# Performance work log

Hardware: AMD Instinct MI355X
Metric: run time of the kernel (lower is better)

The kernel has to match this reference:

```python
import jax, jax.numpy as jnp
import numpy as np

D = 32          # latent_dimension
N = 100000      # num nodes
E = 3200000     # num edges (avg degree 32)
K = 4           # message-passing steps
GAMMA = 0.9
ALPHA = 0.5


def _lin(key, out_f, in_f):
    s = 1.0 / np.sqrt(in_f)
    kw, kb = jax.random.split(key)
    W = jax.random.uniform(kw, (out_f, in_f), minval=-s, maxval=s, dtype=jnp.float32)
    b = jax.random.uniform(kb, (out_f,), minval=-s, maxval=s, dtype=jnp.float32)
    return W, b


def setup_inputs() -> dict:
    key = jax.random.key(0)
    k = iter(jax.random.split(key, 32))
    inp = {}
    inp['x'] = jax.random.normal(next(k), (N, 3), dtype=jnp.float32)
    inp['y'] = jax.random.normal(next(k), (N, 2), dtype=jnp.float32)
    inp['edge_index'] = jax.random.randint(next(k), (2, E), 0, N)
    inp['edge_attr'] = jax.random.uniform(next(k), (E, 2), dtype=jnp.float32)
    inp['to_W1'], inp['to_b1'] = _lin(next(k), D, 2 * D + 2)
    inp['to_W2'], inp['to_b2'] = _lin(next(k), D, D)
    inp['fr_W1'], inp['fr_b1'] = _lin(next(k), D, 2 * D + 2)
    inp['fr_W2'], inp['fr_b2'] = _lin(next(k), D, D)
    inp['lp_W1'], inp['lp_b1'] = _lin(next(k), D, 2 * D + 1)
    inp['lp_W2'], inp['lp_b2'] = _lin(next(k), D, D)
    inp['gru_Wih'], inp['gru_bih'] = _lin(next(k), 3 * D, 4 * D + 3)
    inp['gru_Whh'], inp['gru_bhh'] = _lin(next(k), 3 * D, D)
    inp['dec_W1'], inp['dec_b1'] = _lin(next(k), D, D)
    inp['dec_W2'], inp['dec_b2'] = _lin(next(k), 2, D)
    return inp


def _mlp2(h, W1, b1, W2, b2):
    return jax.nn.relu(h @ W1.T + b1) @ W2.T + b2


def reference(x, y, edge_index, edge_attr,
              to_W1, to_b1, to_W2, to_b2,
              fr_W1, fr_b1, fr_W2, fr_b2,
              lp_W1, lp_b1, lp_W2, lp_b2,
              gru_Wih, gru_bih, gru_Whh, gru_bhh,
              dec_W1, dec_b1, dec_W2, dec_b2):
    n = x.shape[0]
    d = gru_Whh.shape[1]
    src, dst = edge_index[0], edge_index[1]
    nonself = src != dst                     # remove_self_loops in Phi modules
    emask = nonself.astype(x.dtype)          # [E]

    # Loop module: add_self_loops(weight=1), adjacency diagonal = 1 + sum of
    # original self-loop weights (edge_attr[:,0]); loop_col = 1 - diag.
    diag = jnp.ones((n,), x.dtype).at[src].add(
        jnp.where(nonself, jnp.zeros_like(edge_attr[:, 0]), edge_attr[:, 0]))
    loop_col = (1.0 - diag)[:, None]         # [N,1]

    def agg_mean(msg, idx):
        # masked scatter-mean over edges -> nodes; nodes w/o messages get 0
        s = jax.ops.segment_sum(msg * emask[:, None], idx, num_segments=n)
        c = jax.ops.segment_sum(emask, idx, num_segments=n)
        return s / jnp.maximum(c, 1.0)[:, None]

    def gru_step(xin):  # single-step GRU, h0 = 0 (W_hh @ h vanishes)
        g = xin @ gru_Wih.T + gru_bih
        r_x, z_x, n_x = jnp.split(g, 3, axis=-1)
        b_hr, b_hz, b_hn = jnp.split(gru_bhh, 3)
        r = jax.nn.sigmoid(r_x + b_hr)
        z = jax.nn.sigmoid(z_x + b_hz)
        nn_ = jnp.tanh(n_x + r * b_hn)
        return (1.0 - z) * nn_

    def decode(H):
        return _mlp2(H, dec_W1, dec_b1, dec_W2, dec_b2)

    H = jnp.zeros((n, d), x.dtype)
    losses = []
    F = decode(H)
    for _ in range(K):
        h_dst, h_src = H[dst], H[src]
        # Phi_to: flow source_to_target -> x_i = x[dst], x_j = x[src], agg @ dst
        m_to = agg_mean(_mlp2(jnp.concatenate([h_dst, h_src, edge_attr], 1),
                              to_W1, to_b1, to_W2, to_b2), dst)
        # Phi_from: flow target_to_source -> x_i = x[src], x_j = x[dst], agg @ src
        m_fr = agg_mean(_mlp2(jnp.concatenate([h_src, h_dst, edge_attr], 1),
                              fr_W1, fr_b1, fr_W2, fr_b2), src)
        lp = _mlp2(jnp.concatenate([H, H, loop_col], 1), lp_W1, lp_b1, lp_W2, lp_b2)
        concat = jnp.concatenate([H, m_to, m_fr, lp, x], 1)   # [N, 4D+3]
        H = gru_step(concat) * ALPHA + H
        F = decode(H)
        losses.append(jnp.mean((F - y) ** 2))
    losses = jnp.stack(losses)                                # [K]
    weights = GAMMA ** jnp.arange(K - 1, -1, -1, dtype=x.dtype)
    total_loss = jnp.sum(losses * weights)
    return F, total_loss, losses
```

## Files before the change

kernel.cpp:

```cpp
#include <hip/hip_runtime.h>
#include <math.h>


#define BSHIFT 9
#define BIN_W 512
#define CAP 17408
#define EPB 8192

__device__ __forceinline__ unsigned int pack_bf(float x) {
  unsigned int u = __float_as_uint(x);
  u += 0x7fffu + ((u >> 16) & 1u);
  return u >> 16;
}

__global__ void combine_kernel(const float* __restrict__ Wih, const float* __restrict__ bih,
    const float* __restrict__ toW2, const float* __restrict__ tob2,
    const float* __restrict__ frW2, const float* __restrict__ frb2,
    const float* __restrict__ lpW2, const float* __restrict__ lpb2,
    const float* __restrict__ lpW1,
    float* __restrict__ Wg, float* __restrict__ Wlp1c) {
  int tid = blockIdx.x * blockDim.x + threadIdx.x;
  if (tid < 9216) {
    int seg = tid / 3072, r2 = tid % 3072, g = r2 >> 5, j = r2 & 31;
    const float* W2 = seg == 0 ? toW2 : (seg == 1 ? frW2 : lpW2);
    const float* wrow = Wih + g*131 + 32 + seg*32;
    float s = 0.f;
    #pragma unroll
    for (int k = 0; k < 32; k++) s += wrow[k] * W2[k*32 + j];
    int nr = (g & 31)*3 + (g >> 5);
    Wg[nr*136 + 32 + seg*32 + j] = s;
  } else if (tid < 12288) {
    int r2 = tid - 9216, g = r2 >> 5, k = r2 & 31;
    int nr = (g & 31)*3 + (g >> 5);
    Wg[nr*136 + k] = Wih[g*131 + k];
  } else if (tid < 12576) {
    int r2 = tid - 12288; int g = r2 / 3, c = r2 % 3;
    int nr = (g & 31)*3 + (g >> 5);
    Wg[nr*136 + 128 + c] = Wih[g*131 + 128 + c];
  } else if (tid < 12672) {
    int g = tid - 12576;
    float vt = 0.f, vf = 0.f, bl = 0.f;
    #pragma unroll
    for (int k = 0; k < 32; k++) {
      vt += Wih[g*131 + 32 + k] * tob2[k];
      vf += Wih[g*131 + 64 + k] * frb2[k];
      bl += Wih[g*131 + 96 + k] * lpb2[k];
    }
    int nr = (g & 31)*3 + (g >> 5);
    Wg[nr*136 + 131] = bih[g] + bl;
    Wg[nr*136 + 132] = vt;
    Wg[nr*136 + 133] = vf;
  } else if (tid < 13696) {
    int r2 = tid - 12672; int i = r2 >> 5, k = r2 & 31;
    Wlp1c[i*32 + k] = lpW1[i*65 + k] + lpW1[i*65 + 32 + k];
  }
}

__global__ __launch_bounds__(256) void transpose_kernel(
    const float* __restrict__ Wg, const float* __restrict__ toW1,
    const float* __restrict__ frW1, const float* __restrict__ Wlp1c,
    const float* __restrict__ lpW1, const float* __restrict__ lpb1,
    float* __restrict__ Wgt, float* __restrict__ Wc, float* __restrict__ Wtail) {
  int tid = blockIdx.x*256 + threadIdx.x;
  if (tid < 12864) {
    int og = tid / 1608, r = tid % 1608, k = r / 12, jj = r % 12;
    Wgt[(og*134 + k)*16 + jj] = Wg[(og*12 + jj)*136 + k];
  } else if (tid < 12864 + 5120) {
    int r = tid - 12864;
    int og = r / 640, r2 = r % 640, k = r2 / 20, j = r2 % 20;
    int f = og*4 + (j & 3);
    int cls = j >> 2;
    float v;
    if      (cls == 0) v = toW1[f*66 + k];
    else if (cls == 1) v = toW1[f*66 + 32 + k];
    else if (cls == 2) v = frW1[f*66 + k];
    else if (cls == 3) v = frW1[f*66 + 32 + k];
    else               v = Wlp1c[f*32 + k];
    Wc[(og*32 + k)*24 + j] = v;
  } else if (tid < 12864 + 5120 + 64) {
    int f = tid - 12864 - 5120;
    Wtail[f] = (f < 32) ? lpW1[f*65 + 64] : lpb1[f - 32];
  }
}

__global__ __launch_bounds__(1024) void scatter_bin_kernel(
    const int* __restrict__ ei, const float* __restrict__ ea,
    int* __restrict__ cursor_to, int* __restrict__ cursor_fr,
    uint2* __restrict__ binned_to, uint2* __restrict__ binned_fr,
    float* __restrict__ loop_col, int E) {
  __shared__ int lh_to[256], lh_fr[256];
  __shared__ int gb_to[256], gb_fr[256];
  int t = threadIdx.x;
  if (t < 256) { lh_to[t] = 0; lh_fr[t] = 0; }
  __syncthreads();
  int base_e = blockIdx.x * EPB;
  #pragma unroll
  for (int j = 0; j < EPB/1024; j++) {
    int e = base_e + j*1024 + t;
    if (e < E) {
      int ss = ei[e], dd = ei[E + e];
      if (ss != dd) {
        atomicAdd(&lh_to[dd >> BSHIFT], 1);
        atomicAdd(&lh_fr[ss >> BSHIFT], 1);
      } else {
        atomicAdd(&loop_col[ss], -ea[2*e]);
      }
    }
  }
  __syncthreads();
  if (t < 256) {
    int c = lh_to[t]; gb_to[t] = c ? atomicAdd(&cursor_to[t], c) : 0; lh_to[t] = 0;
    c = lh_fr[t];     gb_fr[t] = c ? atomicAdd(&cursor_fr[t], c) : 0; lh_fr[t] = 0;
  }
  __syncthreads();
  #pragma unroll
  for (int j = 0; j < EPB/1024; j++) {
    int e = base_e + j*1024 + t;
    if (e < E) {
      int ss = ei[e], dd = ei[E + e];
      if (ss != dd) {
        float2 a = ((const float2*)ea)[e];
        unsigned int ep = pack_bf(a.x) | (pack_bf(a.y) << 16);
        int bt = dd >> BSHIFT, bf = ss >> BSHIFT;
        int st = gb_to[bt] + atomicAdd(&lh_to[bt], 1);
        int sf = gb_fr[bf] + atomicAdd(&lh_fr[bf], 1);
        if (st < CAP) binned_to[(size_t)bt*CAP + st] =
            make_uint2((unsigned int)ss | ((unsigned int)(dd & 511) << 17), ep);
        if (sf < CAP) binned_fr[(size_t)bf*CAP + sf] =
            make_uint2((unsigned int)dd | ((unsigned int)(ss & 511) << 17), ep);
      }
    }
  }
}

__global__ __launch_bounds__(256) void bin_count_kernel(
    const uint2* __restrict__ binned_to, const int* __restrict__ cursor_to,
    const uint2* __restrict__ binned_fr, const int* __restrict__ cursor_fr,
    int* __restrict__ cnt_dst, int* __restrict__ cnt_src, int NB, int N) {
  __shared__ int c[BIN_W];
  int b = blockIdx.x;
  bool second = b >= NB;
  if (second) b -= NB;
  const uint2* binned = second ? binned_fr : binned_to;
  const int* cursor   = second ? cursor_fr : cursor_to;
  int* cnt            = second ? cnt_src   : cnt_dst;
  for (int i = threadIdx.x; i < BIN_W; i += 256) c[i] = 0;
  __syncthreads();
  int m = cursor[b]; if (m > CAP) m = CAP;
  const uint2* seg = binned + (size_t)b*CAP;
  for (int i = threadIdx.x; i < m; i += 256)
    atomicAdd(&c[seg[i].x >> 17], 1);
  __syncthreads();
  for (int i = threadIdx.x; i < BIN_W; i += 256) {
    int n = (b << BSHIFT) + i;
    if (n < N) cnt[n] = c[i];
  }
}

__global__ __launch_bounds__(256) void scan_part_kernel(
    const int* __restrict__ cnt_a, const int* __restrict__ cnt_b,
    int* __restrict__ part, int n, int G) {
  __shared__ int ws[4];
  int b = blockIdx.x, t = threadIdx.x, lane = t & 63, w = t >> 6;
  int base = b*1024 + t*4;
  for (int which = 0; which < 2; which++) {
    const int* cnt = which ? cnt_b : cnt_a;
    int sum = 0;
    #pragma unroll
    for (int j = 0; j < 4; j++) if (base + j < n) sum += cnt[base + j];
    #pragma unroll
    for (int off = 32; off; off >>= 1) sum += __shfl_down(sum, off, 64);
    if (lane == 0) ws[w] = sum;
    __syncthreads();
    if (t == 0) part[which*G + b] = ws[0] + ws[1] + ws[2] + ws[3];
    __syncthreads();
  }
}

__global__ __launch_bounds__(256) void scan_mid_kernel(
    int* __restrict__ part, int* __restrict__ row_a, int* __restrict__ row_b,
    int n, int G) {
  __shared__ int ws[2][4];
  int t = threadIdx.x, lane = t & 63, w = t >> 6;
  for (int which = 0; which < 2; which++) {
    int v = (t < G) ? part[which*G + t] : 0;
    int orig = v;
    #pragma unroll
    for (int off = 1; off < 64; off <<= 1) {
      int u = __shfl_up(v, off, 64);
      if (lane >= off) v += u;
    }
    if (lane == 63) ws[which][w] = v;
    __syncthreads();
    int wadd = 0;
    for (int i = 0; i < w; i++) wadd += ws[which][i];
    int incl = v + wadd;
    if (t < G) part[which*G + t] = incl - orig;
    if (t == G - 1) { int* row = which ? row_b : row_a; row[n] = incl; }
    __syncthreads();
  }
}

__global__ __launch_bounds__(256) void scan_apply_kernel(
    const int* __restrict__ cnt_a, const int* __restrict__ cnt_b,
    const int* __restrict__ part, int* __restrict__ row_a, int* __restrict__ row_b,
    int n, int G) {
  __shared__ int ws[4];
  int b = blockIdx.x, t = threadIdx.x, lane = t & 63, w = t >> 6;
  int base = b*1024 + t*4;
  for (int which = 0; which < 2; which++) {
    const int* cnt = which ? cnt_b : cnt_a;
    int* row = which ? row_b : row_a;
    int v0 = (base   < n) ? cnt[base]   : 0;
    int v1 = (base+1 < n) ? cnt[base+1] : 0;
    int v2 = (base+2 < n) ? cnt[base+2] : 0;
    int v3 = (base+3 < n) ? cnt[base+3] : 0;
    int tsum = v0 + v1 + v2 + v3;
    int v = tsum;
    #pragma unroll
    for (int off = 1; off < 64; off <<= 1) {
      int u = __shfl_up(v, off, 64);
      if (lane >= off) v += u;
    }
    if (lane == 63) ws[w] = v;
    __syncthreads();
    int wadd = 0;
    for (int i = 0; i < w; i++) wadd += ws[i];
    int excl = v - tsum + wadd + part[which*G + b];
    if (base   < n) row[base]   = excl;
    if (base+1 < n) row[base+1] = excl + v0;
    if (base+2 < n) row[base+2] = excl + v0 + v1;
    if (base+3 < n) row[base+3] = excl + v0 + v1 + v2;
    __syncthreads();
  }
}

__global__ __launch_bounds__(256) void place_kernel(
    const uint2* __restrict__ binned_to, const int* __restrict__ cursor_to,
    const uint2* __restrict__ binned_fr, const int* __restrict__ cursor_fr,
    const int* __restrict__ row_to, const int* __restrict__ row_fr,
    uint2* __restrict__ rec_to, uint2* __restrict__ rec_fr, int NB, int N) {
  __shared__ int cur[BIN_W];
  int b = blockIdx.x;
  bool second = b >= NB;
  if (second) b -= NB;
  const uint2* binned = second ? binned_fr : binned_to;
  const int* cursor   = second ? cursor_fr : cursor_to;
  const int* row      = second ? row_fr    : row_to;
  uint2* rec          = second ? rec_fr    : rec_to;
  int n0 = b << BSHIFT;
  for (int i = threadIdx.x; i < BIN_W; i += 256) {
    int n = n0 + i;
    cur[i] = (n < N) ? row[n] : 0;
  }
  __syncthreads();
  int m = cursor[b]; if (m > CAP) m = CAP;
  const uint2* seg = binned + (size_t)b*CAP;
  for (int i = threadIdx.x; i < m; i += 256) {
    uint2 r = seg[i];
    int pos = atomicAdd(&cur[r.x >> 17], 1);
    rec[pos] = make_uint2((r.x & 0x1ffffu) << 6, r.y);
  }
}

__global__ __launch_bounds__(256) void hlp0_kernel(
    const float* __restrict__ lpW1, const float* __restrict__ lpb1,
    const float* __restrict__ loop_col, float* __restrict__ inX, int N) {
  int tid = blockIdx.x*256 + threadIdx.x;
  int n = tid >> 5, f = tid & 31;
  if (n < N)
    inX[(size_t)n*128 + 96 + f] = fmaxf(lpW1[f*65 + 64]*loop_col[n] + lpb1[f], 0.f);
}

__global__ __launch_bounds__(256) void agg_dual_kernel(
    const float* __restrict__ Pti, const unsigned short* __restrict__ Ptj,
    const int* __restrict__ row_to, const uint2* __restrict__ rec_to,
    const float* __restrict__ toW1, const float* __restrict__ tob1,
    const float* __restrict__ Pfi, const unsigned short* __restrict__ Pfj,
    const int* __restrict__ row_fr, const uint2* __restrict__ rec_fr,
    const float* __restrict__ frW1, const float* __restrict__ frb1,
    float* __restrict__ inX, int skipP, int N) {
  int b = blockIdx.x;
  int low = b & 7;
  bool second = low >= 4;
  int inner = (b >> 3)*4 + (low & 3);
  const float* Pi            = second ? Pfi   : Pti;
  const unsigned short* Pj   = second ? Pfj   : Ptj;
  const int* row             = second ? row_fr: row_to;
  const uint2* rec           = second ? rec_fr: rec_to;
  const float* W1            = second ? frW1  : toW1;
  const float* b1            = second ? frb1  : tob1;
  int slot                   = second ? 64    : 32;
  int t = inner*256 + threadIdx.x;
  int n = t >> 5;
  if (n >= N) return;
  int f = t & 31;
  int start = row[n], end = row[n+1];
  float we0 = W1[f*66 + 64], we1 = W1[f*66 + 65];
  float s = 0.f;
  const char* Pjb = (const char*)Pj;
  unsigned f2 = (unsigned)(f << 1);
  if (skipP) {
    float base = b1[f];
    int i = start;
    if ((i & 1) && i < end) {
      unsigned ep = rec[i].y;
      float e0 = __uint_as_float(ep << 16);
      float e1 = __uint_as_float(ep & 0xffff0000u);
      s += fmaxf(base + we0*e0 + we1*e1, 0.f);
      i++;
    }
    int npair = (end - i) >> 1;
    const uint4* rp4 = (const uint4*)(rec + i);
    #pragma unroll 4
    for (int p = 0; p < npair; p++) {
      uint4 rr = *rp4++;
      float e0a = __uint_as_float(rr.y << 16);
      float e1a = __uint_as_float(rr.y & 0xffff0000u);
      s += fmaxf(base + we0*e0a + we1*e1a, 0.f);
      float e0b = __uint_as_float(rr.w << 16);
      float e1b = __uint_as_float(rr.w & 0xffff0000u);
      s += fmaxf(base + we0*e0b + we1*e1b, 0.f);
    }
    i += npair << 1;
    if (i < end) {
      unsigned ep = rec[i].y;
      float e0 = __uint_as_float(ep << 16);
      float e1 = __uint_as_float(ep & 0xffff0000u);
      s += fmaxf(base + we0*e0 + we1*e1, 0.f);
    }
  } else {
    float base = Pi[n*32 + f] + b1[f];
    int i = start;
    if ((i & 1) && i < end) {
      uint2 r = rec[i];
      float e0 = __uint_as_float(r.y << 16);
      float e1 = __uint_as_float(r.y & 0xffff0000u);
      unsigned pv = *(const unsigned short*)(Pjb + (r.x + f2));
      float pj = __uint_as_float(pv << 16);
      s += fmaxf(base + pj + we0*e0 + we1*e1, 0.f);
      i++;
    }
    int npair = (end - i) >> 1;
    const uint4* rp4 = (const uint4*)(rec + i);
    #pragma unroll 4
    for (int p = 0; p < npair; p++) {
      uint4 rr = *rp4++;
      unsigned pva = *(const unsigned short*)(Pjb + (rr.x + f2));
      unsigned pvb = *(const unsigned short*)(Pjb + (rr.z + f2));
      float e0a = __uint_as_float(rr.y << 16);
      float e1a = __uint_as_float(rr.y & 0xffff0000u);
      float pja = __uint_as_float(pva << 16);
      s += fmaxf(base + pja + we0*e0a + we1*e1a, 0.f);
      float e0b = __uint_as_float(rr.w << 16);
      float e1b = __uint_as_float(rr.w & 0xffff0000u);
      float pjb_ = __uint_as_float(pvb << 16);
      s += fmaxf(base + pjb_ + we0*e0b + we1*e1b, 0.f);
    }
    i += npair << 1;
    if (i < end) {
      uint2 r = rec[i];
      float e0 = __uint_as_float(r.y << 16);
      float e1 = __uint_as_float(r.y & 0xffff0000u);
      unsigned pv = *(const unsigned short*)(Pjb + (r.x + f2));
      float pj = __uint_as_float(pv << 16);
      s += fmaxf(base + pj + we0*e0 + we1*e1, 0.f);
    }
  }
  int c = end - start;
  inX[(size_t)n*128 + slot + f] = s / (float)(c > 0 ? c : 1);
}

__global__ __launch_bounds__(512, 8) void node_update_kernel(
    float* __restrict__ inX, const float* __restrict__ Wgt,
    const float* __restrict__ x, const float* __restrict__ y,
    const int* __restrict__ cnt_dst, const int* __restrict__ cnt_src,
    const float* __restrict__ bhh,
    const float* __restrict__ dW1, const float* __restrict__ db1,
    const float* __restrict__ dW2, const float* __restrict__ db2,
    const float* __restrict__ loop_col,
    const float* __restrict__ Wc, const float* __restrict__ Wtail,
    float* __restrict__ Pti, unsigned short* __restrict__ Ptj,
    float* __restrict__ Pfi, unsigned short* __restrict__ Pfj,
    float* __restrict__ Fout, float* __restrict__ loss_acc, int k_iter, int N) {
  __shared__ float sbuf[64*137];
  __shared__ float sF[1024];
  int t = threadIdx.x;
  int node0 = blockIdx.x * 64;
  {
    const float4* src = (const float4*)(inX + (size_t)node0*128);
    int nvalid = N - node0; if (nvalid > 64) nvalid = 64;
    int nfl4 = nvalid * 32;
    for (int i = t; i < 64*32; i += 512) {
      float4 v = (i < nfl4) ? src[i] : make_float4(0.f, 0.f, 0.f, 0.f);
      int node = i >> 5, k = (i & 31) * 4;
      float* dp = &sbuf[node*137 + k];
      dp[0] = v.x; dp[1] = v.y; dp[2] = v.z; dp[3] = v.w;
    }
    if (t < 64) {
      int n = node0 + t;
      float x0=0.f, x1=0.f, x2=0.f, gt=0.f, gf=0.f;
      if (n < N) {
        x0 = x[n*3]; x1 = x[n*3+1]; x2 = x[n*3+2];
        gt = cnt_dst[n] > 0 ? 1.f : 0.f;
        gf = cnt_src[n] > 0 ? 1.f : 0.f;
      }
      float* dp = &sbuf[t*137 + 128];
      dp[0]=x0; dp[1]=x1; dp[2]=x2; dp[3]=1.f; dp[4]=gt; dp[5]=gf;
    }
  }
  __syncthreads();
  int lane_node = t & 63;
  int og = __builtin_amdgcn_readfirstlane(t >> 6);
  const float* inrow = &sbuf[lane_node*137];
  float acc[12];
  #pragma unroll
  for (int jj = 0; jj < 12; jj++) acc[jj] = 0.f;
  const float* wt = Wgt + og*134*16;
  #pragma unroll 4
  for (int k = 0; k < 134; k++) {
    float iv = inrow[k];
    const float* wk = wt + k*16;
    #pragma unroll
    for (int jj = 0; jj < 12; jj++) acc[jj] += wk[jj] * iv;
  }
  float hnew[4];
  {
    int n = node0 + lane_node;
    #pragma unroll
    for (int q = 0; q < 4; q++) {
      int f = og*4 + q;
      float r = 1.f/(1.f + __expf(-(acc[q*3]   + bhh[f])));
      float z = 1.f/(1.f + __expf(-(acc[q*3+1] + bhh[32+f])));
      float nn = tanhf(acc[q*3+2] + r*bhh[64+f]);
      hnew[q] = (1.f - z)*nn*0.5f + inrow[f];
      if (n < N) inX[(size_t)n*128 + f] = hnew[q];
    }
  }
  __syncthreads();
  #pragma unroll
  for (int q = 0; q < 4; q++) sbuf[lane_node*137 + og*4 + q] = hnew[q];
  __syncthreads();
  float F0p = 0.f, F1p = 0.f;
  #pragma unroll
  for (int q = 0; q < 4; q++) {
    int jd = og*4 + q;
    float a = db1[jd];
    const float* wd = dW1 + jd*32;
    #pragma unroll
    for (int k = 0; k < 32; k++) a += wd[k]*inrow[k];
    a = fmaxf(a, 0.f);
    F0p += dW2[jd]*a;
    F1p += dW2[32+jd]*a;
  }
  sF[t*2] = F0p; sF[t*2+1] = F1p;
  __syncthreads();
  if (k_iter < 3) {
    int n = node0 + lane_node;
    bool valid = n < N;
    float lc = valid ? loop_col[n] : 0.f;
    int fb = og*4;
    float a[20];
    #pragma unroll
    for (int j = 0; j < 20; j++) a[j] = 0.f;
    const float* wc = Wc + og*32*24;
    #pragma unroll 2
    for (int k = 0; k < 32; k++) {
      float hk = inrow[k];
      const float* wck = wc + k*24;
      #pragma unroll
      for (int j = 0; j < 20; j++) a[j] += wck[j] * hk;
    }
    if (valid) {
      *(float4*)&Pti[(size_t)n*32 + fb] = make_float4(a[0],a[1],a[2],a[3]);
      uint2 u;
      u.x = pack_bf(a[4]) | (pack_bf(a[5]) << 16);
      u.y = pack_bf(a[6]) | (pack_bf(a[7]) << 16);
      *(uint2*)&Ptj[(size_t)n*32 + fb] = u;
      *(float4*)&Pfi[(size_t)n*32 + fb] = make_float4(a[8],a[9],a[10],a[11]);
      u.x = pack_bf(a[12]) | (pack_bf(a[13]) << 16);
      u.y = pack_bf(a[14]) | (pack_bf(a[15]) << 16);
      *(uint2*)&Pfj[(size_t)n*32 + fb] = u;
      float hl[4];
      #pragma unroll
      for (int q = 0; q < 4; q++)
        hl[q] = fmaxf(a[16+q] + Wtail[fb+q]*lc + Wtail[32+fb+q], 0.f);
      *(float4*)&inX[(size_t)n*128 + 96 + fb] = make_float4(hl[0],hl[1],hl[2],hl[3]);
    }
  }
  float my_loss = 0.f;
  if (og == 0) {
    int n = node0 + lane_node;
    float F0 = db2[0], F1 = db2[1];
    #pragma unroll
    for (int w = 0; w < 8; w++) {
      F0 += sF[(t + 64*w)*2];
      F1 += sF[(t + 64*w)*2 + 1];
    }
    if (n < N) {
      ((float2*)Fout)[n] = make_float2(F0, F1);
      float e0 = F0 - y[n*2], e1 = F1 - y[n*2+1];
      my_loss = e0*e0 + e1*e1;
    }
  }
  #pragma unroll
  for (int off = 32; off > 0; off >>= 1) my_loss += __shfl_down(my_loss, off, 64);
  if (t == 0) atomicAdd(&loss_acc[k_iter], my_loss);
}

__global__ void finalize_kernel(const float* __restrict__ loss_acc, float* __restrict__ out, int N) {
  if (threadIdx.x == 0 && blockIdx.x == 0) {
    float inv = 1.f/(2.f*(float)N);
    float l0 = loss_acc[0]*inv, l1 = loss_acc[1]*inv, l2 = loss_acc[2]*inv, l3 = loss_acc[3]*inv;
    out[0] = l0*0.729f + l1*0.81f + l2*0.9f + l3;
    out[1] = l0; out[2] = l1; out[3] = l2; out[4] = l3;
  }
}

extern "C" void kernel_launch(void* const* d_in, const int* in_sizes, int n_in,
                              void* d_out, int out_size, void* d_ws, size_t ws_size,
                              hipStream_t stream) {
  const float* x    = (const float*)d_in[0];
  const float* y    = (const float*)d_in[1];
  const int*   ei   = (const int*)  d_in[2];
  const float* ea   = (const float*)d_in[3];
  const float* toW1 = (const float*)d_in[4];  const float* tob1 = (const float*)d_in[5];
  const float* toW2 = (const float*)d_in[6];  const float* tob2 = (const float*)d_in[7];
  const float* frW1 = (const float*)d_in[8];  const float* frb1 = (const float*)d_in[9];
  const float* frW2 = (const float*)d_in[10]; const float* frb2 = (const float*)d_in[11];
  const float* lpW1 = (const float*)d_in[12]; const float* lpb1 = (const float*)d_in[13];
  const float* lpW2 = (const float*)d_in[14]; const float* lpb2 = (const float*)d_in[15];
  const float* gWih = (const float*)d_in[16]; const float* gbih = (const float*)d_in[17];
  const float* gbhh = (const float*)d_in[19];
  const float* dW1  = (const float*)d_in[20]; const float* db1  = (const float*)d_in[21];
  const float* dW2  = (const float*)d_in[22]; const float* db2  = (const float*)d_in[23];
  const int N = in_sizes[0] / 3;
  const int E = in_sizes[3] / 2;
  const int NB = (N + BIN_W - 1) >> BSHIFT;
  const int G  = (N + 1023) >> 10;

  char* p = (char*)d_ws;
  auto carve = [&](size_t bytes) -> void* {
    void* r = (void*)p;
    p += (bytes + 255) & ~(size_t)255;
    return r;
  };
  float* inX       = (float*)carve((size_t)N*128*4);
  float* loop_col  = (float*)carve((size_t)N*4);
  int*   cursor_to = (int*)  carve((size_t)NB*4);
  int*   cursor_fr = (int*)  carve((size_t)NB*4);
  float* loss_acc  = (float*)carve(64);
  size_t zero_bytes = (size_t)(p - (char*)d_ws);
  int*    row_to   = (int*)  carve((size_t)(N+1)*4);
  int*    row_fr   = (int*)  carve((size_t)(N+1)*4);
  int*    cnt_dst  = (int*)  carve((size_t)N*4);
  int*    cnt_src  = (int*)  carve((size_t)N*4);
  int*    part     = (int*)  carve((size_t)2*G*4);
  uint2*  binned_to= (uint2*)carve((size_t)NB*CAP*8);
  uint2*  binned_fr= (uint2*)carve((size_t)NB*CAP*8);
  uint2*  rec_to   = (uint2*)carve((size_t)E*8);
  uint2*  rec_fr   = (uint2*)carve((size_t)E*8);
  float*  Pti      = (float*)carve((size_t)N*32*4);
  float*  Pfi      = (float*)carve((size_t)N*32*4);
  unsigned short* Ptj = (unsigned short*)carve((size_t)N*32*2);
  unsigned short* Pfj = (unsigned short*)carve((size_t)N*32*2);
  float*  Wg       = (float*)carve((size_t)96*136*4);
  float*  Wlp1c    = (float*)carve(32*32*4);
  float*  Wgt      = (float*)carve((size_t)8*134*16*4);
  float*  Wc       = (float*)carve((size_t)8*32*24*4);
  float*  Wtail    = (float*)carve(64*4);

  hipMemsetAsync(d_ws, 0, zero_bytes, stream);
  combine_kernel<<<54, 256, 0, stream>>>(gWih, gbih, toW2, tob2, frW2, frb2, lpW2, lpb2,
                                         lpW1, Wg, Wlp1c);
  transpose_kernel<<<71, 256, 0, stream>>>(Wg, toW1, frW1, Wlp1c, lpW1, lpb1,
                                           Wgt, Wc, Wtail);
  scatter_bin_kernel<<<(E+EPB-1)/EPB, 1024, 0, stream>>>(ei, ea, cursor_to, cursor_fr,
                                                         binned_to, binned_fr, loop_col, E);
  bin_count_kernel<<<2*NB, 256, 0, stream>>>(binned_to, cursor_to, binned_fr, cursor_fr,
                                             cnt_dst, cnt_src, NB, N);
  scan_part_kernel<<<G, 256, 0, stream>>>(cnt_dst, cnt_src, part, N, G);
  scan_mid_kernel<<<1, 256, 0, stream>>>(part, row_to, row_fr, N, G);
  scan_apply_kernel<<<G, 256, 0, stream>>>(cnt_dst, cnt_src, part, row_to, row_fr, N, G);
  place_kernel<<<2*NB, 256, 0, stream>>>(binned_to, cursor_to, binned_fr, cursor_fr,
                                         row_to, row_fr, rec_to, rec_fr, NB, N);
  hlp0_kernel<<<(N*32 + 255)/256, 256, 0, stream>>>(lpW1, lpb1, loop_col, inX, N);

  float* Fout     = (float*)d_out;
  float* loss_out = (float*)d_out + (size_t)N*2;

  int aggHalf = (N*32 + 255)/256;
  int aggHalf4 = (aggHalf + 3) & ~3;
  for (int k = 0; k < 4; k++) {
    agg_dual_kernel<<<2*aggHalf4, 256, 0, stream>>>(Pti, Ptj, row_to, rec_to, toW1, tob1,
                                                    Pfi, Pfj, row_fr, rec_fr, frW1, frb1,
                                                    inX, (k == 0) ? 1 : 0, N);
    node_update_kernel<<<(N+63)/64, 512, 0, stream>>>(inX, Wgt, x, y,
        cnt_dst, cnt_src, gbhh, dW1, db1, dW2, db2,
        loop_col, Wc, Wtail,
        Pti, Ptj, Pfi, Pfj, Fout, loss_acc, k, N);
  }
  finalize_kernel<<<1, 64, 0, stream>>>(loss_acc, loss_out, N);
}
```

Baseline: 1.021 ms.

## Fuse edge aggregation into node update kernel with double-buffered projections

Merges the separate per-iteration aggregation kernel into the node update kernel, so each block gathers messages for its 64 nodes directly into shared memory instead of writing them to inX and reading them back. Because blocks now read neighbour projections while other blocks write new ones, the projection buffers are double-buffered, with the second set carved out of the no-longer-needed binning scratch space. This removes a launch and the inX round trip per iteration. The cost is less parallelism for the gather: 16 warps per block walk 4 nodes each serially, and register or occupancy pressure in one large kernel may rise.

Measured after the change: 1.069 ms. +4.8%, slower.

```diff
diff --git a/kernel.cpp b/kernel.cpp
--- a/kernel.cpp
+++ b/kernel.cpp
@@ -272,106 +272,7 @@
     inX[(size_t)n*128 + 96 + f] = fmaxf(lpW1[f*65 + 64]*loop_col[n] + lpb1[f], 0.f);
 }
 
-__global__ __launch_bounds__(256) void agg_dual_kernel(
-    const float* __restrict__ Pti, const unsigned short* __restrict__ Ptj,
-    const int* __restrict__ row_to, const uint2* __restrict__ rec_to,
-    const float* __restrict__ toW1, const float* __restrict__ tob1,
-    const float* __restrict__ Pfi, const unsigned short* __restrict__ Pfj,
-    const int* __restrict__ row_fr, const uint2* __restrict__ rec_fr,
-    const float* __restrict__ frW1, const float* __restrict__ frb1,
-    float* __restrict__ inX, int skipP, int N) {
-  int b = blockIdx.x;
-  int low = b & 7;
-  bool second = low >= 4;
-  int inner = (b >> 3)*4 + (low & 3);
-  const float* Pi            = second ? Pfi   : Pti;
-  const unsigned short* Pj   = second ? Pfj   : Ptj;
-  const int* row             = second ? row_fr: row_to;
-  const uint2* rec           = second ? rec_fr: rec_to;
-  const float* W1            = second ? frW1  : toW1;
-  const float* b1            = second ? frb1  : tob1;
-  int slot                   = second ? 64    : 32;
-  int t = inner*256 + threadIdx.x;
-  int n = t >> 5;
-  if (n >= N) return;
-  int f = t & 31;
-  int start = row[n], end = row[n+1];
-  float we0 = W1[f*66 + 64], we1 = W1[f*66 + 65];
-  float s = 0.f;
-  const char* Pjb = (const char*)Pj;
-  unsigned f2 = (unsigned)(f << 1);
-  if (skipP) {
-    float base = b1[f];
-    int i = start;
-    if ((i & 1) && i < end) {
-      unsigned ep = rec[i].y;
-      float e0 = __uint_as_float(ep << 16);
-      float e1 = __uint_as_float(ep & 0xffff0000u);
-      s += fmaxf(base + we0*e0 + we1*e1, 0.f);
-      i++;
-    }
-    int npair = (end - i) >> 1;
-    const uint4* rp4 = (const uint4*)(rec + i);
-    #pragma unroll 4
-    for (int p = 0; p < npair; p++) {
-      uint4 rr = *rp4++;
-      float e0a = __uint_as_float(rr.y << 16);
-      float e1a = __uint_as_float(rr.y & 0xffff0000u);
-      s += fmaxf(base + we0*e0a + we1*e1a, 0.f);
-      float e0b = __uint_as_float(rr.w << 16);
-      float e1b = __uint_as_float(rr.w & 0xffff0000u);
-      s += fmaxf(base + we0*e0b + we1*e1b, 0.f);
-    }
-    i += npair << 1;
-    if (i < end) {
-      unsigned ep = rec[i].y;
-      float e0 = __uint_as_float(ep << 16);
-      float e1 = __uint_as_float(ep & 0xffff0000u);
-      s += fmaxf(base + we0*e0 + we1*e1, 0.f);
-    }
-  } else {
-    float base = Pi[n*32 + f] + b1[f];
-    int i = start;
-    if ((i & 1) && i < end) {
-      uint2 r = rec[i];
-      float e0 = __uint_as_float(r.y << 16);
-      float e1 = __uint_as_float(r.y & 0xffff0000u);
-      unsigned pv = *(const unsigned short*)(Pjb + (r.x + f2));
-      float pj = __uint_as_float(pv << 16);
-      s += fmaxf(base + pj + we0*e0 + we1*e1, 0.f);
-      i++;
-    }
-    int npair = (end - i) >> 1;
-    const uint4* rp4 = (const uint4*)(rec + i);
-    #pragma unroll 4
-    for (int p = 0; p < npair; p++) {
-      uint4 rr = *rp4++;
-      unsigned pva = *(const unsigned short*)(Pjb + (rr.x + f2));
-      unsigned pvb = *(const unsigned short*)(Pjb + (rr.z + f2));
-      float e0a = __uint_as_float(rr.y << 16);
-      float e1a = __uint_as_float(rr.y & 0xffff0000u);
-      float pja = __uint_as_float(pva << 16);
-      s += fmaxf(base + pja + we0*e0a + we1*e1a, 0.f);
-      float e0b = __uint_as_float(rr.w << 16);
-      float e1b = __uint_as_float(rr.w & 0xffff0000u);
-      float pjb_ = __uint_as_float(pvb << 16);
-      s += fmaxf(base + pjb_ + we0*e0b + we1*e1b, 0.f);
-    }
-    i += npair << 1;
-    if (i < end) {
-      uint2 r = rec[i];
-      float e0 = __uint_as_float(r.y << 16);
-      float e1 = __uint_as_float(r.y & 0xffff0000u);
-      unsigned pv = *(const unsigned short*)(Pjb + (r.x + f2));
-      float pj = __uint_as_float(pv << 16);
-      s += fmaxf(base + pj + we0*e0 + we1*e1, 0.f);
-    }
-  }
-  int c = end - start;
-  inX[(size_t)n*128 + slot + f] = s / (float)(c > 0 ? c : 1);
-}
-
-__global__ __launch_bounds__(512, 8) void node_update_kernel(
+__global__ __launch_bounds__(512, 8) void fused_iter_kernel(
     float* __restrict__ inX, const float* __restrict__ Wgt,
     const float* __restrict__ x, const float* __restrict__ y,
     const int* __restrict__ cnt_dst, const int* __restrict__ cnt_src,
@@ -380,22 +281,30 @@
     const float* __restrict__ dW2, const float* __restrict__ db2,
     const float* __restrict__ loop_col,
     const float* __restrict__ Wc, const float* __restrict__ Wtail,
-    float* __restrict__ Pti, unsigned short* __restrict__ Ptj,
-    float* __restrict__ Pfi, unsigned short* __restrict__ Pfj,
-    float* __restrict__ Fout, float* __restrict__ loss_acc, int k_iter, int N) {
+    const float* __restrict__ PtiR, const unsigned short* __restrict__ PtjR,
+    const float* __restrict__ PfiR, const unsigned short* __restrict__ PfjR,
+    const int* __restrict__ row_to, const uint2* __restrict__ rec_to,
+    const int* __restrict__ row_fr, const uint2* __restrict__ rec_fr,
+    const float* __restrict__ toW1, const float* __restrict__ tob1,
+    const float* __restrict__ frW1, const float* __restrict__ frb1,
+    float* __restrict__ PtiW, unsigned short* __restrict__ PtjW,
+    float* __restrict__ PfiW, unsigned short* __restrict__ PfjW,
+    float* __restrict__ Fout, float* __restrict__ loss_acc,
+    int skipP, int k_iter, int N) {
   __shared__ float sbuf[64*137];
   __shared__ float sF[1024];
   int t = threadIdx.x;
   int node0 = blockIdx.x * 64;
   {
-    const float4* src = (const float4*)(inX + (size_t)node0*128);
     int nvalid = N - node0; if (nvalid > 64) nvalid = 64;
-    int nfl4 = nvalid * 32;
-    for (int i = t; i < 64*32; i += 512) {
-      float4 v = (i < nfl4) ? src[i] : make_float4(0.f, 0.f, 0.f, 0.f);
-      int node = i >> 5, k = (i & 31) * 4;
-      float* dp = &sbuf[node*137 + k];
-      dp[0] = v.x; dp[1] = v.y; dp[2] = v.z; dp[3] = v.w;
+    for (int i = t; i < 1024; i += 512) {
+      int node = i >> 4, kq = i & 15;
+      int k4 = kq < 8 ? kq : kq + 16;
+      float4 v = (node < nvalid)
+          ? ((const float4*)(inX + (size_t)(node0+node)*128))[k4]
+          : make_float4(0.f, 0.f, 0.f, 0.f);
+      float* dp = &sbuf[node*137 + k4*4];
+      dp[0]=v.x; dp[1]=v.y; dp[2]=v.z; dp[3]=v.w;
     }
     if (t < 64) {
       int n = node0 + t;
@@ -407,6 +316,94 @@
       }
       float* dp = &sbuf[t*137 + 128];
       dp[0]=x0; dp[1]=x1; dp[2]=x2; dp[3]=1.f; dp[4]=gt; dp[5]=gf;
+    }
+  }
+  __syncthreads();
+  {
+    int lane_f = t & 31;
+    int grp = t >> 5;
+    unsigned f2 = (unsigned)(lane_f << 1);
+    #pragma unroll 1
+    for (int dir = 0; dir < 2; dir++) {
+      const float* Pi            = dir ? PfiR  : PtiR;
+      const unsigned short* Pj   = dir ? PfjR  : PtjR;
+      const int* row             = dir ? row_fr: row_to;
+      const uint2* rec           = dir ? rec_fr: rec_to;
+      const float* W1            = dir ? frW1  : toW1;
+      const float* b1            = dir ? frb1  : tob1;
+      int slot                   = dir ? 64    : 32;
+      const char* Pjb = (const char*)Pj;
+      float we0 = W1[lane_f*66 + 64], we1 = W1[lane_f*66 + 65];
+      float bb = b1[lane_f];
+      #pragma unroll 1
+      for (int step = 0; step < 4; step++) {
+        int nd = step*16 + grp;
+        int n = node0 + nd;
+        if (n >= N) continue;
+        int start = row[n], end = row[n+1];
+        float s = 0.f;
+        if (skipP) {
+          float base = bb;
+          int i = start;
+          if ((i & 1) && i < end) {
+            unsigned ep = rec[i].y;
+            s += fmaxf(base + we0*__uint_as_float(ep << 16)
+                            + we1*__uint_as_float(ep & 0xffff0000u), 0.f);
+            i++;
+          }
+          int npair = (end - i) >> 1;
+          const uint4* rp4 = (const uint4*)(rec + i);
+          #pragma unroll 4
+          for (int p = 0; p < npair; p++) {
+            uint4 rr = *rp4++;
+            s += fmaxf(base + we0*__uint_as_float(rr.y << 16)
+                            + we1*__uint_as_float(rr.y & 0xffff0000u), 0.f);
+            s += fmaxf(base + we0*__uint_as_float(rr.w << 16)
+                            + we1*__uint_as_float(rr.w & 0xffff0000u), 0.f);
+          }
+          i += npair << 1;
+          if (i < end) {
+            unsigned ep = rec[i].y;
+            s += fmaxf(base + we0*__uint_as_float(ep << 16)
+                            + we1*__uint_as_float(ep & 0xffff0000u), 0.f);
+          }
+        } else {
+          float base = Pi[n*32 + lane_f] + bb;
+          int i = start;
+          if ((i & 1) && i < end) {
+            uint2 r = rec[i];
+            unsigned pv = *(const unsigned short*)(Pjb + (r.x + f2));
+            s += fmaxf(base + __uint_as_float(pv << 16)
+                            + we0*__uint_as_float(r.y << 16)
+                            + we1*__uint_as_float(r.y & 0xffff0000u), 0.f);
+            i++;
+          }
+          int npair = (end - i) >> 1;
+          const uint4* rp4 = (const uint4*)(rec + i);
+          #pragma unroll 4
+          for (int p = 0; p < npair; p++) {
+            uint4 rr = *rp4++;
+            unsigned pva = *(const unsigned short*)(Pjb + (rr.x + f2));
+            unsigned pvb = *(const unsigned short*)(Pjb + (rr.z + f2));
+            s += fmaxf(base + __uint_as_float(pva << 16)
+                            + we0*__uint_as_float(rr.y << 16)
+                            + we1*__uint_as_float(rr.y & 0xffff0000u), 0.f);
+            s += fmaxf(base + __uint_as_float(pvb << 16)
+                            + we0*__uint_as_float(rr.w << 16)
+                            + we1*__uint_as_float(rr.w & 0xffff0000u), 0.f);
+          }
+          i += npair << 1;
+          if (i < end) {
+            uint2 r = rec[i];
+            unsigned pv = *(const unsigned short*)(Pjb + (r.x + f2));
+            s += fmaxf(base + __uint_as_float(pv << 16)
+                            + we0*__uint_as_float(r.y << 16)
+                            + we1*__uint_as_float(r.y & 0xffff0000u), 0.f);
+          }
+        }
+        int c = end - start;
+        sbuf[nd*137 + slot + lane_f] = s / (float)(c > 0 ? c : 1);
+      }
     }
   }
   __syncthreads();
@@ -472,15 +469,15 @@
       for (int j = 0; j < 20; j++) a[j] += wck[j] * hk;
     }
     if (valid) {
-      *(float4*)&Pti[(size_t)n*32 + fb] = make_float4(a[0],a[1],a[2],a[3]);
+      *(float4*)&PtiW[(size_t)n*32 + fb] = make_float4(a[0],a[1],a[2],a[3]);
       uint2 u;
       u.x = pack_bf(a[4]) | (pack_bf(a[5]) << 16);
       u.y = pack_bf(a[6]) | (pack_bf(a[7]) << 16);
-      *(uint2*)&Ptj[(size_t)n*32 + fb] = u;
-      *(float4*)&Pfi[(size_t)n*32 + fb] = make_float4(a[8],a[9],a[10],a[11]);
+      *(uint2*)&PtjW[(size_t)n*32 + fb] = u;
+      *(float4*)&PfiW[(size_t)n*32 + fb] = make_float4(a[8],a[9],a[10],a[11]);
       u.x = pack_bf(a[12]) | (pack_bf(a[13]) << 16);
       u.y = pack_bf(a[14]) | (pack_bf(a[15]) << 16);
-      *(uint2*)&Pfj[(size_t)n*32 + fb] = u;
+      *(uint2*)&PfjW[(size_t)n*32 + fb] = u;
       float hl[4];
       #pragma unroll
       for (int q = 0; q < 4; q++)
@@ -560,15 +557,25 @@
   uint2*  binned_fr= (uint2*)carve((size_t)NB*CAP*8);
   uint2*  rec_to   = (uint2*)carve((size_t)E*8);
   uint2*  rec_fr   = (uint2*)carve((size_t)E*8);
-  float*  Pti      = (float*)carve((size_t)N*32*4);
-  float*  Pfi      = (float*)carve((size_t)N*32*4);
-  unsigned short* Ptj = (unsigned short*)carve((size_t)N*32*2);
-  unsigned short* Pfj = (unsigned short*)carve((size_t)N*32*2);
+  float*  Pti0     = (float*)carve((size_t)N*32*4);
+  float*  Pfi0     = (float*)carve((size_t)N*32*4);
+  unsigned short* Ptj0 = (unsigned short*)carve((size_t)N*32*2);
+  unsigned short* Pfj0 = (unsigned short*)carve((size_t)N*32*2);
   float*  Wg       = (float*)carve((size_t)96*136*4);
   float*  Wlp1c    = (float*)carve(32*32*4);
   float*  Wgt      = (float*)carve((size_t)8*134*16*4);
   float*  Wc       = (float*)carve((size_t)8*32*24*4);
   float*  Wtail    = (float*)carve(64*4);
+  char* pb = (char*)binned_to;
+  auto carve2 = [&](size_t bytes) -> void* {
+    void* r = (void*)pb;
+    pb += (bytes + 255) & ~(size_t)255;
+    return r;
+  };
+  float*  Pti1     = (float*)carve2((size_t)N*32*4);
+  float*  Pfi1     = (float*)carve2((size_t)N*32*4);
+  unsigned short* Ptj1 = (unsigned short*)carve2((size_t)N*32*2);
+  unsigned short* Pfj1 = (unsigned short*)carve2((size_t)N*32*2);
 
   hipMemsetAsync(d_ws, 0, zero_bytes, stream);
   combine_kernel<<<54, 256, 0, stream>>>(gWih, gbih, toW2, tob2, frW2, frb2, lpW2, lpb2,
@@ -589,16 +596,21 @@
   float* Fout     = (float*)d_out;
   float* loss_out = (float*)d_out + (size_t)N*2;
 
-  int aggHalf = (N*32 + 255)/256;
-  int aggHalf4 = (aggHalf + 3) & ~3;
   for (int k = 0; k < 4; k++) {
-    agg_dual_kernel<<<2*aggHalf4, 256, 0, stream>>>(Pti, Ptj, row_to, rec_to, toW1, tob1,
-                                                    Pfi, Pfj, row_fr, rec_fr, frW1, frb1,
-                                                    inX, (k == 0) ? 1 : 0, N);
-    node_update_kernel<<<(N+63)/64, 512, 0, stream>>>(inX, Wgt, x, y,
-        cnt_dst, cnt_src, gbhh, dW1, db1, dW2, db2,
-        loop_col, Wc, Wtail,
-        Pti, Ptj, Pfi, Pfj, Fout, loss_acc, k, N);
+    const float* PtiR = (k & 1) ? Pti1 : Pti0;
+    const float* PfiR = (k & 1) ? Pfi1 : Pfi0;
+    const unsigned short* PtjR = (k & 1) ? Ptj1 : Ptj0;
+    const unsigned short* PfjR = (k & 1) ? Pfj1 : Pfj0;
+    float* PtiW = (k & 1) ? Pti0 : Pti1;
+    float* PfiW = (k & 1) ? Pfi0 : Pfi1;
+    unsigned short* PtjW = (k & 1) ? Ptj0 : Ptj1;
+    unsigned short* PfjW = (k & 1) ? Pfj0 : Pfj1;
+    fused_iter_kernel<<<(N+63)/64, 512, 0, stream>>>(inX, Wgt, x, y,
+        cnt_dst, cnt_src, gbhh, dW1, db1, dW2, db2, loop_col, Wc, Wtail,
+        PtiR, PtjR, PfiR, PfjR, row_to, rec_to, row_fr, rec_fr,
+        toW1, tob1, frW1, frb1,
+        PtiW, PtjW, PfiW, PfjW,
+        Fout, loss_acc, (k == 0) ? 1 : 0, k, N);
   }
   finalize_kernel<<<1, 64, 0, stream>>>(loss_acc, loss_out, N);
 }
```
